# Performance work log

Hardware: AMD Instinct MI355X
Metric: run time of the kernel (lower is better)

The kernel has to match this reference:

```python
import jax, jax.numpy as jnp
import numpy as np

N = 100000        # nodes per batch
B = 1             # batch_size
E = 3200000       # edges
IN_F = 128        # in_features
ATT = 128         # attention_dim
HEADS = 8
DK = ATT // HEADS
SLOPE = 0.2       # leaky_relu_slope


def setup_inputs() -> dict:
    key = jax.random.key(0)
    k1, k2, k3, k4 = jax.random.split(key, 4)
    x = jax.random.normal(k1, (B * N, IN_F), dtype=jnp.float32)
    edge = jax.random.randint(k2, (B, 2, E), 0, N)
    # xavier_normal with gain=1.414 on W:[IN_F, ATT]
    W = jax.random.normal(k3, (IN_F, ATT), dtype=jnp.float32) * (1.414 * np.sqrt(2.0 / (IN_F + ATT)))
    # a originally [1, 2*d_k, 1, 1]; flattened to [2*d_k] (same math)
    a = jax.random.normal(k4, (2 * DK,), dtype=jnp.float32) * (1.414 * np.sqrt(2.0 / (2 * DK + 1)))
    return {"x": x, "edge": edge, "W": W, "a": a}


def _segment_softmax(scores, seg):
    # scores: [E, H], seg: [E] -> softmax within each segment (node id)
    smax = jax.ops.segment_max(scores, seg, num_segments=N)
    ex = jnp.exp(scores - smax[seg])
    denom = jax.ops.segment_sum(ex, seg, num_segments=N)
    return ex / denom[seg]


def reference(x, edge, W, a):
    wx = x @ W                                           # [B*N, ATT]
    h = wx.reshape(B, N, HEADS, DK).transpose(0, 1, 3, 2)  # [B, N, DK, H]
    a1, a2 = a[:DK], a[DK:]
    # sum(a * concat(h_src, h_dst)) = a1.h_src + a2.h_dst (linearity)
    s_src = jnp.einsum('bnkh,k->bnh', h, a1)             # [B, N, H]
    s_dst = jnp.einsum('bnkh,k->bnh', h, a2)             # [B, N, H]
    src = edge[:, 0, :]                                  # [B, E]
    dst = edge[:, 1, :]                                  # [B, E]
    gather = jax.vmap(lambda s, i: s[i])
    scores = gather(s_src, src) + gather(s_dst, dst)     # [B, E, H]
    edge_e = jnp.where(scores > 0, scores, SLOPE * scores)  # leaky relu
    # attention_norm_idx = 0 -> normalize over edges sharing a source node
    attention = jax.vmap(_segment_softmax)(edge_e, src)  # [B, E, H]
    return attention, wx
```

## Files before the change

### kernel.cpp

```cpp
#include <hip/hip_runtime.h>

#define N_NODES 100000
#define E_EDGES 3200000
#define IN_F 128
#define ATT 128
#define HEADS 8
#define DK 16
#define SLOPE 0.2f
#define NH (N_NODES * HEADS)

#define CHUNK 896
#define NBINS 112
#define NS 8
#define HB 512
#define EPB 6272

__global__ __launch_bounds__(256) void gemm_s_kernel(
    const float* __restrict__ x, const float* __restrict__ W,
    const float* __restrict__ a, float* __restrict__ wx,
    float* __restrict__ s_src, float* __restrict__ s_dst)
{
    __shared__ float xs[8][128];
    __shared__ float Ws[8][128];

    const int tid = threadIdx.x;
    const int ty  = tid >> 4;
    const int tx  = tid & 15;
    const int row0 = blockIdx.x * 128;

    float acc[8][8];
#pragma unroll
    for (int i = 0; i < 8; i++)
#pragma unroll
        for (int j = 0; j < 8; j++) acc[i][j] = 0.f;

    const int lrow  = tid >> 1;
    const int khalf = (tid & 1) * 4;
    const int wkk   = tid >> 5;
    const int wc    = (tid & 31) * 4;

    for (int k0 = 0; k0 < IN_F; k0 += 8) {
        float4 xv = make_float4(0.f, 0.f, 0.f, 0.f);
        const int grow = row0 + lrow;
        if (grow < N_NODES)
            xv = *(const float4*)(x + (size_t)grow * IN_F + k0 + khalf);
        const float4 wv = *(const float4*)(W + (size_t)(k0 + wkk) * ATT + wc);

        __syncthreads();
        xs[khalf + 0][lrow] = xv.x;
        xs[khalf + 1][lrow] = xv.y;
        xs[khalf + 2][lrow] = xv.z;
        xs[khalf + 3][lrow] = xv.w;
        *(float4*)(&Ws[wkk][wc]) = wv;
        __syncthreads();

#pragma unroll
        for (int kk = 0; kk < 8; kk++) {
            float av[8], bv[8];
            *(float4*)(av)     = *(const float4*)(&xs[kk][ty * 8]);
            *(float4*)(av + 4) = *(const float4*)(&xs[kk][ty * 8 + 4]);
            *(float4*)(bv)     = *(const float4*)(&Ws[kk][tx * 8]);
            *(float4*)(bv + 4) = *(const float4*)(&Ws[kk][tx * 8 + 4]);
#pragma unroll
            for (int r = 0; r < 8; r++)
#pragma unroll
                for (int c = 0; c < 8; c++)
                    acc[r][c] = fmaf(av[r], bv[c], acc[r][c]);
        }
    }

    const int koff = (tx & 1) * 8;
    const int head = tx >> 1;
    float a1[8], a2[8];
#pragma unroll
    for (int c = 0; c < 8; c++) {
        a1[c] = a[koff + c];
        a2[c] = a[DK + koff + c];
    }

#pragma unroll
    for (int r = 0; r < 8; r++) {
        const int grow = row0 + ty * 8 + r;
        const bool ok = (grow < N_NODES);
        if (ok) {
            *(float4*)(wx + (size_t)grow * ATT + tx * 8) =
                make_float4(acc[r][0], acc[r][1], acc[r][2], acc[r][3]);
            *(float4*)(wx + (size_t)grow * ATT + tx * 8 + 4) =
                make_float4(acc[r][4], acc[r][5], acc[r][6], acc[r][7]);
        }
        float p1 = 0.f, p2 = 0.f;
#pragma unroll
        for (int c = 0; c < 8; c++) {
            p1 = fmaf(acc[r][c], a1[c], p1);
            p2 = fmaf(acc[r][c], a2[c], p2);
        }
        p1 += __shfl_xor(p1, 1);
        p2 += __shfl_xor(p2, 1);
        if (((tx & 1) == 0) && ok) {
            s_src[(size_t)grow * HEADS + head] = p1;
            s_dst[(size_t)grow * HEADS + head] = p2;
        }
    }
}

__global__ __launch_bounds__(256) void hist_kernel(
    const int* __restrict__ src, int* __restrict__ counts)
{
    __shared__ int h[NBINS];
    const int t = threadIdx.x;
    const int b = blockIdx.x;
    for (int i = t; i < NBINS; i += 256) h[i] = 0;
    __syncthreads();

    const int rb = b * EPB;
    const int re = min(rb + EPB, E_EDGES);
    for (int i = rb + t * 4; i < re; i += 256 * 4) {
        const int4 s4 = *(const int4*)(src + i);
        atomicAdd(&h[s4.x / CHUNK], 1);
        atomicAdd(&h[s4.y / CHUNK], 1);
        atomicAdd(&h[s4.z / CHUNK], 1);
        atomicAdd(&h[s4.w / CHUNK], 1);
    }
    __syncthreads();
    for (int i = t; i < NBINS; i += 256) counts[i * HB + b] = h[i];
}

__global__ __launch_bounds__(1024) void scan_kernel(
    const int* __restrict__ counts, int* __restrict__ offs)
{
    __shared__ int part[1024];
    const int t = threadIdx.x;
    const int per = (NBINS * HB) / 1024;
    const int base = t * per;

    int sum = 0;
    for (int i = 0; i < per; i++) sum += counts[base + i];
    part[t] = sum;
    __syncthreads();

    for (int off = 1; off < 1024; off <<= 1) {
        int v = 0;
        if (t >= off) v = part[t - off];
        __syncthreads();
        if (t >= off) part[t] += v;
        __syncthreads();
    }

    int run = (t == 0) ? 0 : part[t - 1];
    for (int i = 0; i < per; i++) {
        offs[base + i] = run;
        run += counts[base + i];
    }
}

__global__ __launch_bounds__(256) void scatter_kernel(
    const int* __restrict__ src, const int* __restrict__ dst,
    const int* __restrict__ offs, unsigned int* __restrict__ binned)
{
    __shared__ int cur[NBINS];
    const int t = threadIdx.x;
    const int b = blockIdx.x;
    for (int i = t; i < NBINS; i += 256) cur[i] = offs[i * HB + b];
    __syncthreads();

    const int rb = b * EPB;
    const int re = min(rb + EPB, E_EDGES);
    for (int i = rb + t * 4; i < re; i += 256 * 4) {
        const int4 s4 = *(const int4*)(src + i);
        const int4 d4 = *(const int4*)(dst + i);
        const int ss[4] = {s4.x, s4.y, s4.z, s4.w};
        const int dd[4] = {d4.x, d4.y, d4.z, d4.w};
#pragma unroll
        for (int j = 0; j < 4; j++) {
            const int c = ss[j] / CHUNK;
            const int pos = atomicAdd(&cur[c], 1);
            binned[pos] = ((unsigned int)(ss[j] - c * CHUNK) << 17) |
                          (unsigned int)dd[j];
        }
    }
}

__global__ __launch_bounds__(256, 4) void denom_binned_kernel(
    const unsigned int* __restrict__ binned, const int* __restrict__ offs,
    const float* __restrict__ s_src, const float* __restrict__ s_dst,
    float* __restrict__ denoms)
{
    __shared__ float acc[HEADS][CHUNK + 1];

    const int t  = threadIdx.x;
    const int c  = blockIdx.x;
    const int j  = blockIdx.y;
    const int lo = c * CHUNK;
    const int hi = min(lo + CHUNK, N_NODES);

    for (int i = t; i < HEADS * (CHUNK + 1); i += 256)
        ((float*)acc)[i] = 0.f;
    __syncthreads();

    const int start = offs[c * HB];
    const int end   = (c + 1 < NBINS) ? offs[(c + 1) * HB] : E_EDGES;
    const int len   = end - start;
    const int e0 = start + (int)((long long)len * j / NS);
    const int e1 = start + (int)((long long)len * (j + 1) / NS);

    int i = e0 + t;
    for (; i + 256 < e1; i += 512) {
        const unsigned int w0 = binned[i];
        const unsigned int w1 = binned[i + 256];
        const int di0 = w0 & 0x1FFFF, sl0 = w0 >> 17;
        const int di1 = w1 & 0x1FFFF, sl1 = w1 >> 17;
        const float4* ps0 = (const float4*)(s_src + (size_t)(lo + sl0) * HEADS);
        const float4* pd0 = (const float4*)(s_dst + (size_t)di0 * HEADS);
        const float4* ps1 = (const float4*)(s_src + (size_t)(lo + sl1) * HEADS);
        const float4* pd1 = (const float4*)(s_dst + (size_t)di1 * HEADS);
        const float4 xa0 = ps0[0], xa1 = ps0[1], xb0 = pd0[0], xb1 = pd0[1];
        const float4 ya0 = ps1[0], ya1 = ps1[1], yb0 = pd1[0], yb1 = pd1[1];
        const float s0[8] = {xa0.x + xb0.x, xa0.y + xb0.y, xa0.z + xb0.z, xa0.w + xb0.w,
                             xa1.x + xb1.x, xa1.y + xb1.y, xa1.z + xb1.z, xa1.w + xb1.w};
        const float s1[8] = {ya0.x + yb0.x, ya0.y + yb0.y, ya0.z + yb0.z, ya0.w + yb0.w,
                             ya1.x + yb1.x, ya1.y + yb1.y, ya1.z + yb1.z, ya1.w + yb1.w};
#pragma unroll
        for (int h = 0; h < 8; h++) {
            float v0 = s0[h]; v0 = v0 > 0.f ? v0 : SLOPE * v0;
            float v1 = s1[h]; v1 = v1 > 0.f ? v1 : SLOPE * v1;
            atomicAdd(&acc[h][sl0], __expf(v0));
            atomicAdd(&acc[h][sl1], __expf(v1));
        }
    }
    if (i < e1) {
        const unsigned int w0 = binned[i];
        const int di0 = w0 & 0x1FFFF, sl0 = w0 >> 17;
        const float4* ps0 = (const float4*)(s_src + (size_t)(lo + sl0) * HEADS);
        const float4* pd0 = (const float4*)(s_dst + (size_t)di0 * HEADS);
        const float4 xa0 = ps0[0], xa1 = ps0[1], xb0 = pd0[0], xb1 = pd0[1];
        const float s0[8] = {xa0.x + xb0.x, xa0.y + xb0.y, xa0.z + xb0.z, xa0.w + xb0.w,
                             xa1.x + xb1.x, xa1.y + xb1.y, xa1.z + xb1.z, xa1.w + xb1.w};
#pragma unroll
        for (int h = 0; h < 8; h++) {
            float v0 = s0[h]; v0 = v0 > 0.f ? v0 : SLOPE * v0;
            atomicAdd(&acc[h][sl0], __expf(v0));
        }
    }
    __syncthreads();

    const int cnt = (hi - lo) * HEADS;
    float* outp = denoms + (size_t)j * NH + (size_t)lo * HEADS;
    for (int i2 = t; i2 < cnt; i2 += 256)
        outp[i2] = acc[i2 & 7][i2 >> 3];
}

__global__ __launch_bounds__(256) void reduce_recip_kernel(float* __restrict__ denoms)
{
    const int i = blockIdx.x * 256 + threadIdx.x;
    if (i >= NH) return;
    float s = 0.f;
#pragma unroll
    for (int c = 0; c < NS; c++) s += denoms[(size_t)c * NH + i];
    denoms[i] = __frcp_rn(s);
}

__global__ __launch_bounds__(256) void norm_kernel(
    const int* __restrict__ src, const int* __restrict__ dst,
    const float* __restrict__ s_src, const float* __restrict__ s_dst,
    const float* __restrict__ rdenom, float* __restrict__ att)
{
    const int e = blockIdx.x * 256 + threadIdx.x;
    if (e >= E_EDGES) return;
    const int s = src[e];
    const int d = dst[e];
    const float4* ps = (const float4*)(s_src + (size_t)s * HEADS);
    const float4* pd = (const float4*)(s_dst + (size_t)d * HEADS);
    const float4 s0 = ps[0], s1 = ps[1], d0 = pd[0], d1 = pd[1];
    const float4* pr = (const float4*)(rdenom + (size_t)s * HEADS);
    const float4 r0 = pr[0], r1 = pr[1];
    float sc[8] = {s0.x + d0.x, s0.y + d0.y, s0.z + d0.z, s0.w + d0.w,
                   s1.x + d1.x, s1.y + d1.y, s1.z + d1.z, s1.w + d1.w};
    float rd[8] = {r0.x, r0.y, r0.z, r0.w, r1.x, r1.y, r1.z, r1.w};
    float o[8];
#pragma unroll
    for (int h = 0; h < 8; h++) {
        float v = sc[h];
        v = v > 0.f ? v : SLOPE * v;
        o[h] = __expf(v) * rd[h];
    }
    float4* po = (float4*)(att + (size_t)e * HEADS);
    po[0] = make_float4(o[0], o[1], o[2], o[3]);
    po[1] = make_float4(o[4], o[5], o[6], o[7]);
}

extern "C" void kernel_launch(void* const* d_in, const int* in_sizes, int n_in,
                              void* d_out, int out_size, void* d_ws, size_t ws_size,
                              hipStream_t stream)
{
    const float* x    = (const float*)d_in[0];
    const int*   edge = (const int*)d_in[1];
    const float* W    = (const float*)d_in[2];
    const float* a    = (const float*)d_in[3];

    float* out = (float*)d_out;
    float* att = out;
    float* wx  = out + (size_t)E_EDGES * HEADS;

    float* ws     = (float*)d_ws;
    float* s_src  = ws;
    float* s_dst  = s_src + (size_t)NH;
    float* denoms = s_dst + (size_t)NH;
    int*   counts = (int*)(denoms + (size_t)NS * NH);
    int*   offs   = counts + (size_t)NBINS * HB;

    unsigned int* binned = (unsigned int*)att;

    const int* src = edge;
    const int* dst = edge + E_EDGES;

    const int gemm_blocks = (N_NODES + 127) / 128;
    gemm_s_kernel<<<gemm_blocks, 256, 0, stream>>>(x, W, a, wx, s_src, s_dst);

    hist_kernel<<<HB, 256, 0, stream>>>(src, counts);
    scan_kernel<<<1, 1024, 0, stream>>>(counts, offs);
    scatter_kernel<<<HB, 256, 0, stream>>>(src, dst, offs, binned);

    dim3 bgrid(NBINS, NS);
    denom_binned_kernel<<<bgrid, 256, 0, stream>>>(binned, offs, s_src, s_dst, denoms);

    const int nblocks = (NH + 255) / 256;
    reduce_recip_kernel<<<nblocks, 256, 0, stream>>>(denoms);

    const int eblocks = (E_EDGES + 255) / 256;
    norm_kernel<<<eblocks, 256, 0, stream>>>(src, dst, s_src, s_dst, denoms, att);
}
```

Measured before the change: 551.0 us.

## Halve denom bin size, double occupancy, prefetch binned words, vectorize output

Shrinks each source-node chunk from 896 to 448 nodes, doubling the number of bins and halving the per-block shared accumulator so eight blocks per CU can be resident. Restructures the edge loop to software-prefetch the next pair of packed edge words while the current pair's gathers and LDS atomics run, and folds the tail iteration into the main loop. Writes the per-node head sums as two float4 stores instead of scalar strided stores. The costs are more blocks and more partial outputs to reduce, and the 8-blocks-per-CU launch bound may constrain registers.

```diff
diff --git a/kernel.cpp b/kernel.cpp
--- a/kernel.cpp
+++ b/kernel.cpp
@@ -9,8 +9,8 @@
 #define SLOPE 0.2f
 #define NH (N_NODES * HEADS)
 
-#define CHUNK 896
-#define NBINS 112
+#define CHUNK 448
+#define NBINS 224
 #define NS 8
 #define HB 512
 #define EPB 6272
@@ -180,7 +180,7 @@
     }
 }
 
-__global__ __launch_bounds__(256, 4) void denom_binned_kernel(
+__global__ __launch_bounds__(256, 8) void denom_binned_kernel(
     const unsigned int* __restrict__ binned, const int* __restrict__ offs,
     const float* __restrict__ s_src, const float* __restrict__ s_dst,
     float* __restrict__ denoms)
@@ -204,9 +204,22 @@
     const int e1 = start + (int)((long long)len * (j + 1) / NS);
 
     int i = e0 + t;
-    for (; i + 256 < e1; i += 512) {
-        const unsigned int w0 = binned[i];
-        const unsigned int w1 = binned[i + 256];
+    bool v0 = i < e1;
+    bool v1 = i + 256 < e1;
+    unsigned int pw0 = v0 ? binned[i] : 0u;
+    unsigned int pw1 = v1 ? binned[i + 256] : 0u;
+
+    while (v0) {
+        const unsigned int w0 = pw0;
+        const unsigned int w1 = v1 ? pw1 : pw0;
+        const bool cv1 = v1;
+
+        i += 512;
+        v0 = i < e1;
+        v1 = i + 256 < e1;
+        if (v0) pw0 = binned[i];
+        if (v1) pw1 = binned[i + 256];
+
         const int di0 = w0 & 0x1FFFF, sl0 = w0 >> 17;
         const int di1 = w1 & 0x1FFFF, sl1 = w1 >> 17;
         const float4* ps0 = (const float4*)(s_src + (size_t)(lo + sl0) * HEADS);
@@ -221,32 +234,26 @@
                              ya1.x + yb1.x, ya1.y + yb1.y, ya1.z + yb1.z, ya1.w + yb1.w};
 #pragma unroll
         for (int h = 0; h < 8; h++) {
-            float v0 = s0[h]; v0 = v0 > 0.f ? v0 : SLOPE * v0;
-            float v1 = s1[h]; v1 = v1 > 0.f ? v1 : SLOPE * v1;
-            atomicAdd(&acc[h][sl0], __expf(v0));
-            atomicAdd(&acc[h][sl1], __expf(v1));
-        }
-    }
-    if (i < e1) {
-        const unsigned int w0 = binned[i];
-        const int di0 = w0 & 0x1FFFF, sl0 = w0 >> 17;
-        const float4* ps0 = (const float4*)(s_src + (size_t)(lo + sl0) * HEADS);
-        const float4* pd0 = (const float4*)(s_dst + (size_t)di0 * HEADS);
-        const float4 xa0 = ps0[0], xa1 = ps0[1], xb0 = pd0[0], xb1 = pd0[1];
-        const float s0[8] = {xa0.x + xb0.x, xa0.y + xb0.y, xa0.z + xb0.z, xa0.w + xb0.w,
-                             xa1.x + xb1.x, xa1.y + xb1.y, xa1.z + xb1.z, xa1.w + xb1.w};
-#pragma unroll
-        for (int h = 0; h < 8; h++) {
-            float v0 = s0[h]; v0 = v0 > 0.f ? v0 : SLOPE * v0;
-            atomicAdd(&acc[h][sl0], __expf(v0));
-        }
-    }
-    __syncthreads();
-
-    const int cnt = (hi - lo) * HEADS;
+            float v = s0[h]; v = v > 0.f ? v : SLOPE * v;
+            atomicAdd(&acc[h][sl0], __expf(v));
+        }
+        if (cv1) {
+#pragma unroll
+            for (int h = 0; h < 8; h++) {
+                float v = s1[h]; v = v > 0.f ? v : SLOPE * v;
+                atomicAdd(&acc[h][sl1], __expf(v));
+            }
+        }
+    }
+    __syncthreads();
+
     float* outp = denoms + (size_t)j * NH + (size_t)lo * HEADS;
-    for (int i2 = t; i2 < cnt; i2 += 256)
-        outp[i2] = acc[i2 & 7][i2 >> 3];
+    for (int nd = t; nd < hi - lo; nd += 256) {
+        const float4 o0 = make_float4(acc[0][nd], acc[1][nd], acc[2][nd], acc[3][nd]);
+        const float4 o1 = make_float4(acc[4][nd], acc[5][nd], acc[6][nd], acc[7][nd]);
+        *(float4*)(outp + (size_t)nd * 8)     = o0;
+        *(float4*)(outp + (size_t)nd * 8 + 4) = o1;
+    }
 }
 
 __global__ __launch_bounds__(256) void reduce_recip_kernel(float* __restrict__ denoms)
```

Result: no change. 557.1 us (+1.1%).
